# Kernel optimization log

Measured on AMD Instinct MI355X. Metric: run time of the kernel, lower is better.

## Reference

```python
import jax, jax.numpy as jnp
import numpy as np
from functools import partial

BANK = 256
ADDR = 64
OUT_C, IN_C, KH, KW = 64, 64, 3, 3
BS, H, W = 32, 128, 128


def setup_inputs() -> dict:
    key = jax.random.key(0)
    ks = jax.random.split(key, 6)
    x = jax.random.normal(ks[0], (BS, IN_C, H, W), dtype=jnp.float32)
    w_addr = jax.random.normal(ks[1], (BS, ADDR), dtype=jnp.float32)
    b_addr = jax.random.normal(ks[2], (BS, OUT_C, ADDR), dtype=jnp.float32)
    # learned parameters
    w_bank = jax.random.normal(ks[3], (BANK, OUT_C, IN_C, KH, KW), dtype=jnp.float32) * (1.0 / np.sqrt(IN_C * KH * KW))
    bound = 1.0 / np.sqrt(IN_C * KH * KW)
    b_bank = jax.random.uniform(ks[4], (BANK,), minval=-bound, maxval=bound, dtype=jnp.float32)
    address_space = jax.random.normal(ks[5], (BANK, ADDR), dtype=jnp.float32)
    return {"x": x, "w_addr": w_addr, "b_addr": b_addr, "w_bank": w_bank,
            "b_bank": b_bank, "address_space": address_space, "s": 1, "p": 1}


def _hyper_conv(x, w_addr, b_addr, w_bank, b_bank, address_space, s, p):
    # soft addressing: keys @ address_space.T -> softmax -> weighted sum of bank
    sel_w = jax.nn.softmax(w_addr @ address_space.T, axis=-1)          # [bs, bank]
    w = jnp.einsum('bn,noikl->boikl', sel_w, w_bank)                   # [bs, O, I, kh, kw]
    sel_b = jax.nn.softmax(b_addr @ address_space.T, axis=-1)          # [bs, O, bank]
    b = jnp.einsum('bon,n->bo', sel_b, b_bank)                         # [bs, O]

    def conv_one(xi, wi):
        # xi: [I, H, W], wi: [O, I, kh, kw]
        return jax.lax.conv_general_dilated(
            xi[None], wi, window_strides=(s, s), padding=[(p, p), (p, p)],
            dimension_numbers=('NCHW', 'OIHW', 'NCHW'))[0]

    o = jax.vmap(conv_one)(x, w)                                       # [bs, O, H', W']
    return o + b[:, :, None, None]


def reference(x, w_addr, b_addr, w_bank, b_bank, address_space, s, p):
    return _hyper_conv(x, w_addr, b_addr, w_bank, b_bank, address_space, int(s), int(p))
```

## Files before the change

kernel.cpp:

```cpp
#include <hip/hip_runtime.h>
#include <hip/hip_bf16.h>
#include <math.h>

#define BS   32
#define IC   64
#define OC   64
#define HH   128
#define WW   128
#define BANK 256
#define ADDR 64
#define WELEM (OC*IC*9)
#define PLANE (HH*WW)

typedef short short8 __attribute__((ext_vector_type(8)));
typedef float f32x16 __attribute__((ext_vector_type(16)));

__device__ __forceinline__ short f2bf(float f) {
    unsigned u = __builtin_bit_cast(unsigned, f);
    unsigned r = (u + 0x7FFFu + ((u >> 16) & 1u)) >> 16;
    return (short)r;
}

__global__ __launch_bounds__(BANK) void k_selw(const float* __restrict__ w_addr,
                                               const float* __restrict__ aspace,
                                               float* __restrict__ sel_w) {
    int b = blockIdx.x;
    int n = threadIdx.x;
    const float* wa = w_addr + b * ADDR;
    const float* as = aspace + n * ADDR;
    float dot = 0.f;
#pragma unroll
    for (int k = 0; k < ADDR; ++k) dot = fmaf(wa[k], as[k], dot);

    __shared__ float red[BANK];
    red[n] = dot; __syncthreads();
    for (int s = BANK / 2; s > 0; s >>= 1) {
        if (n < s) red[n] = fmaxf(red[n], red[n + s]);
        __syncthreads();
    }
    float m = red[0]; __syncthreads();
    float e = expf(dot - m);
    red[n] = e; __syncthreads();
    for (int s = BANK / 2; s > 0; s >>= 1) {
        if (n < s) red[n] += red[n + s];
        __syncthreads();
    }
    sel_w[b * BANK + n] = e / red[0];
}

__global__ __launch_bounds__(BANK) void k_bias(const float* __restrict__ b_addr,
                                               const float* __restrict__ aspace,
                                               const float* __restrict__ b_bank,
                                               float* __restrict__ bias) {
    int bo = blockIdx.x;
    int n  = threadIdx.x;
    const float* ba = b_addr + (size_t)bo * ADDR;
    const float* as = aspace + n * ADDR;
    float dot = 0.f;
#pragma unroll
    for (int k = 0; k < ADDR; ++k) dot = fmaf(ba[k], as[k], dot);

    __shared__ float red[BANK];
    red[n] = dot; __syncthreads();
    for (int s = BANK / 2; s > 0; s >>= 1) {
        if (n < s) red[n] = fmaxf(red[n], red[n + s]);
        __syncthreads();
    }
    float m = red[0]; __syncthreads();
    float e = expf(dot - m);
    red[n] = e; __syncthreads();
    for (int s = BANK / 2; s > 0; s >>= 1) {
        if (n < s) red[n] += red[n + s];
        __syncthreads();
    }
    float denom = red[0]; __syncthreads();
    red[n] = e * b_bank[n]; __syncthreads();
    for (int s = BANK / 2; s > 0; s >>= 1) {
        if (n < s) red[n] += red[n + s];
        __syncthreads();
    }
    if (n == 0) bias[bo] = red[0] / denom;
}

__global__ __launch_bounds__(256) void k_wmix(const float* __restrict__ sel_w,
                                              const float* __restrict__ w_bank,
                                              __hip_bfloat16* __restrict__ wmb) {
    __shared__ float s_red[4 * 32 * 64];

    int tid = threadIdx.x;
    int jl  = tid & 63;
    int c   = tid >> 6;
    int jb  = blockIdx.x * 64 + jl;

    int n0 = __builtin_amdgcn_readfirstlane(c * 64);
    const float* selp = sel_w + n0;

    float wv[64];
#pragma unroll
    for (int n = 0; n < 64; ++n)
        wv[n] = w_bank[(size_t)(n0 + n) * WELEM + jb];

    float acc[BS];
#pragma unroll
    for (int b = 0; b < BS; ++b) acc[b] = 0.f;
#pragma unroll
    for (int b = 0; b < BS; ++b)
#pragma unroll
        for (int n = 0; n < 64; ++n)
            acc[b] = fmaf(selp[b * BANK + n], wv[n], acc[b]);

#pragma unroll
    for (int b = 0; b < BS; ++b)
        s_red[(c * 32 + b) * 64 + jl] = acc[b];
    __syncthreads();

    int B0  = (tid * 8) & 31;
    int jl2 = (tid * 8) >> 5;
    int j   = blockIdx.x * 64 + jl2;
    int o   = j / 576;
    int rem = j - o * 576;
    int i   = rem / 9;
    int tap = rem - i * 9;
    size_t base = ((size_t)tap * 8 + (i >> 3)) * 512 + (size_t)o * 8 + (i & 7);
#pragma unroll
    for (int u = 0; u < 8; ++u) {
        int b = B0 + u;
        float v = s_red[(0 * 32 + b) * 64 + jl2] + s_red[(1 * 32 + b) * 64 + jl2]
                + s_red[(2 * 32 + b) * 64 + jl2] + s_red[(3 * 32 + b) * 64 + jl2];
        short sv = f2bf(v);
        wmb[(size_t)b * (9 * 8 * 64 * 8) + base] = *reinterpret_cast<__hip_bfloat16*>(&sv);
    }
}

__global__ __launch_bounds__(512, 4) void k_conv(const float* __restrict__ x,
                                                 const short* __restrict__ wmb,
                                                 const float* __restrict__ bias,
                                                 float* __restrict__ out) {
    __shared__ short s_x[2][4 * 2 * 132 * 8];
    __shared__ short s_w[2][9 * 2 * 64 * 8];
    __shared__ float s_bias[OC];

    int orig    = blockIdx.x;
    int logical = (orig & 7) * 256 + (orig >> 3);
    int b    = logical >> 6;
    int y0   = (logical & 63) * 2;
    int tid  = threadIdx.x;
    int lane = tid & 63;
    int wv   = tid >> 6;
    int h    = lane >> 5;
    int ln   = lane & 31;
    int wr   = wv & 1;
    int oh   = (wv >> 1) & 1;
    int ph   = wv >> 2;

    if (tid < OC) s_bias[tid] = bias[b * OC + tid];
    if (tid < 32) {
        int bf   = tid >> 4;
        int kg   = (tid >> 1) & 7;
        int col  = (tid & 1) ? 129 : 0;
        *(short8*)&s_x[bf][(kg * 132 + col) * 8] = (short8){0,0,0,0,0,0,0,0};
    }

    const float* xb   = x + (size_t)b * IC * PLANE;
    const short* wmbs = wmb + (size_t)b * 36864;

    int x_goff[2], x_lds[2]; bool x_ok[2]; int x_g[2];
#pragma unroll
    for (int k = 0; k < 2; ++k) {
        int u  = k * 512 + tid;
        int ky = u >> 8;
        int g  = (u >> 7) & 1;
        int cx = u & 127;
        int gy = y0 - 1 + ky;
        x_ok[k]   = ((unsigned)gy < (unsigned)HH);
        x_g[k]    = g;
        x_goff[k] = gy * WW + cx;
        x_lds[k]  = ((ky * 2 + g) * 132 + cx + 1) * 8;
    }
    bool w_val[3]; int w_tap[3], w_g[3], w_oc[3];
#pragma unroll
    for (int k = 0; k < 3; ++k) {
        int v = k * 512 + tid;
        w_val[k] = (v < 1152);
        int vv = w_val[k] ? v : 0;
        w_tap[k] = vv >> 7; w_g[k] = (vv >> 6) & 1; w_oc[k] = vv & 63;
    }

    float  xr[2][8];
    short8 wreg[3];

    auto LOAD = [&](int cc) {
#pragma unroll
        for (int k = 0; k < 2; ++k) {
            if (x_ok[k]) {
                const float* p = xb + (size_t)(cc * 16 + x_g[k] * 8) * PLANE + x_goff[k];
#pragma unroll
                for (int e = 0; e < 8; ++e) xr[k][e] = p[(size_t)e * PLANE];
            } else {
#pragma unroll
                for (int e = 0; e < 8; ++e) xr[k][e] = 0.f;
            }
        }
#pragma unroll
        for (int k = 0; k < 3; ++k)
            if (w_val[k])
                wreg[k] = *(const short8*)(wmbs +
                    (size_t)((w_tap[k] * 8 + 2 * cc + w_g[k]) * 64 + w_oc[k]) * 8);
    };
    auto STORE = [&](int bf) {
#pragma unroll
        for (int k = 0; k < 2; ++k) {
            short8 s;
#pragma unroll
            for (int e = 0; e < 8; ++e) s[e] = f2bf(xr[k][e]);
            *(short8*)&s_x[bf][x_lds[k]] = s;
        }
#pragma unroll
        for (int k = 0; k < 3; ++k)
            if (w_val[k])
                *(short8*)&s_w[bf][((w_tap[k] * 2 + w_g[k]) * 64 + w_oc[k]) * 8] = wreg[k];
    };

    f32x16 acc[2];
    acc[0] = (f32x16)0.0f;
    acc[1] = (f32x16)0.0f;

    LOAD(0);
    STORE(0);
    __syncthreads();

#pragma unroll
    for (int cc = 0; cc < 4; ++cc) {
        int bf = cc & 1;
        if (cc < 3) LOAD(cc + 1);
        const short8* xb8 = (const short8*)s_x[bf];
        const short8* wb8 = (const short8*)s_w[bf];
#pragma unroll
        for (int ky = 0; ky < 3; ++ky) {
#pragma unroll
            for (int kx = 0; kx < 3; ++kx) {
                short8 a = wb8[((ky * 3 + kx) * 2 + h) * 64 + oh * 32 + ln];
#pragma unroll
                for (int nt = 0; nt < 2; ++nt) {
                    short8 bb = xb8[((wr + ky) * 2 + h) * 132 + ph * 64 + nt * 32 + ln + kx];
                    acc[nt] = __builtin_amdgcn_mfma_f32_32x32x16_bf16(a, bb, acc[nt], 0, 0, 0);
                }
            }
        }
        if (cc < 3) STORE(bf ^ 1);
        __syncthreads();
    }

    int y = y0 + wr;
    float* ob = out + (size_t)b * OC * PLANE;
#pragma unroll
    for (int nt = 0; nt < 2; ++nt) {
#pragma unroll
        for (int r = 0; r < 16; ++r) {
            int oc = oh * 32 + (r & 3) + 8 * (r >> 2) + 4 * h;
            int px = ph * 64 + nt * 32 + ln;
            ob[((size_t)oc * HH + y) * WW + px] = acc[nt][r] + s_bias[oc];
        }
    }
}

extern "C" void kernel_launch(void* const* d_in, const int* in_sizes, int n_in,
                              void* d_out, int out_size, void* d_ws, size_t ws_size,
                              hipStream_t stream) {
    const float* x      = (const float*)d_in[0];
    const float* w_addr = (const float*)d_in[1];
    const float* b_addr = (const float*)d_in[2];
    const float* w_bank = (const float*)d_in[3];
    const float* b_bank = (const float*)d_in[4];
    const float* aspace = (const float*)d_in[5];
    float* out = (float*)d_out;

    char* ws = (char*)d_ws;
    float*          sel_w = (float*)ws;
    float*          bias  = (float*)(ws + 32768);
    __hip_bfloat16* wmb   = (__hip_bfloat16*)(ws + 40960);

    k_selw<<<BS, BANK, 0, stream>>>(w_addr, aspace, sel_w);
    k_bias<<<BS * OC, BANK, 0, stream>>>(b_addr, aspace, b_bank, bias);
    k_wmix<<<WELEM / 64, 256, 0, stream>>>(sel_w, w_bank, wmb);
    k_conv<<<BS * 64, 512, 0, stream>>>(x, (const short*)wmb, bias, out);
}
```

Before: 133.2 us.

## Split conv tiles into half-width blocks with register-held weights and single LDS buffer

The conv kernel now uses 256-thread blocks that each cover two rows and half the image width, launching twice as many blocks. Weight fragments are read straight from global memory into registers per channel chunk instead of being staged in LDS. The double-buffered LDS pipeline is replaced by a single buffer with two barriers per chunk. The aim is to cut LDS use and raise occupancy, at the cost of more halo reloading of x, more redundant weight fetches and loss of load/compute overlap.

```diff
diff --git a/kernel.cpp b/kernel.cpp
--- a/kernel.cpp
+++ b/kernel.cpp
@@ -132,123 +132,104 @@
     }
 }
 
-__global__ __launch_bounds__(512, 4) void k_conv(const float* __restrict__ x,
+__global__ __launch_bounds__(256, 4) void k_conv(const float* __restrict__ x,
                                                  const short* __restrict__ wmb,
                                                  const float* __restrict__ bias,
                                                  float* __restrict__ out) {
-    __shared__ short s_x[2][4 * 2 * 132 * 8];
-    __shared__ short s_w[2][9 * 2 * 64 * 8];
+    __shared__ short s_x[4 * 2 * 66 * 8];
     __shared__ float s_bias[OC];
 
     int orig    = blockIdx.x;
-    int logical = (orig & 7) * 256 + (orig >> 3);
-    int b    = logical >> 6;
-    int y0   = (logical & 63) * 2;
+    int logical = (orig & 7) * 512 + (orig >> 3);
+    int b    = logical >> 7;
+    int rem  = logical & 127;
+    int y0   = (rem >> 1) * 2;
+    int ch   = rem & 1;
     int tid  = threadIdx.x;
     int lane = tid & 63;
     int wv   = tid >> 6;
     int h    = lane >> 5;
     int ln   = lane & 31;
     int wr   = wv & 1;
-    int oh   = (wv >> 1) & 1;
-    int ph   = wv >> 2;
+    int oh   = wv >> 1;
 
     if (tid < OC) s_bias[tid] = bias[b * OC + tid];
-    if (tid < 32) {
-        int bf   = tid >> 4;
-        int kg   = (tid >> 1) & 7;
-        int col  = (tid & 1) ? 129 : 0;
-        *(short8*)&s_x[bf][(kg * 132 + col) * 8] = (short8){0,0,0,0,0,0,0,0};
-    }
 
     const float* xb   = x + (size_t)b * IC * PLANE;
     const short* wmbs = wmb + (size_t)b * 36864;
 
-    int x_goff[2], x_lds[2]; bool x_ok[2]; int x_g[2];
-#pragma unroll
-    for (int k = 0; k < 2; ++k) {
-        int u  = k * 512 + tid;
-        int ky = u >> 8;
-        int g  = (u >> 7) & 1;
-        int cx = u & 127;
+    int x_goff[3], x_lds[3], x_g[3]; bool x_ok[3];
+#pragma unroll
+    for (int k = 0; k < 3; ++k) {
+        int u = k * 256 + tid;
+        bool val = (u < 528);
+        int uu = val ? u : 0;
+        int ky = uu / 132;
+        int r  = uu - ky * 132;
+        int g  = r / 66;
+        int cx = r - g * 66;
         int gy = y0 - 1 + ky;
-        x_ok[k]   = ((unsigned)gy < (unsigned)HH);
+        int gx = ch * 64 - 1 + cx;
+        x_ok[k]   = val && ((unsigned)gy < (unsigned)HH) && ((unsigned)gx < (unsigned)WW);
         x_g[k]    = g;
-        x_goff[k] = gy * WW + cx;
-        x_lds[k]  = ((ky * 2 + g) * 132 + cx + 1) * 8;
-    }
-    bool w_val[3]; int w_tap[3], w_g[3], w_oc[3];
-#pragma unroll
-    for (int k = 0; k < 3; ++k) {
-        int v = k * 512 + tid;
-        w_val[k] = (v < 1152);
-        int vv = w_val[k] ? v : 0;
-        w_tap[k] = vv >> 7; w_g[k] = (vv >> 6) & 1; w_oc[k] = vv & 63;
-    }
-
-    float  xr[2][8];
-    short8 wreg[3];
-
-    auto LOAD = [&](int cc) {
-#pragma unroll
-        for (int k = 0; k < 2; ++k) {
-            if (x_ok[k]) {
-                const float* p = xb + (size_t)(cc * 16 + x_g[k] * 8) * PLANE + x_goff[k];
-#pragma unroll
-                for (int e = 0; e < 8; ++e) xr[k][e] = p[(size_t)e * PLANE];
-            } else {
-#pragma unroll
-                for (int e = 0; e < 8; ++e) xr[k][e] = 0.f;
-            }
-        }
-#pragma unroll
-        for (int k = 0; k < 3; ++k)
-            if (w_val[k])
-                wreg[k] = *(const short8*)(wmbs +
-                    (size_t)((w_tap[k] * 8 + 2 * cc + w_g[k]) * 64 + w_oc[k]) * 8);
-    };
-    auto STORE = [&](int bf) {
-#pragma unroll
-        for (int k = 0; k < 2; ++k) {
-            short8 s;
-#pragma unroll
-            for (int e = 0; e < 8; ++e) s[e] = f2bf(xr[k][e]);
-            *(short8*)&s_x[bf][x_lds[k]] = s;
-        }
-#pragma unroll
-        for (int k = 0; k < 3; ++k)
-            if (w_val[k])
-                *(short8*)&s_w[bf][((w_tap[k] * 2 + w_g[k]) * 64 + w_oc[k]) * 8] = wreg[k];
-    };
+        x_goff[k] = gy * WW + gx;
+        x_lds[k]  = val ? ((ky * 2 + g) * 66 + cx) * 8 : (528 * 8);
+        if (!val) x_lds[k] = 0;
+        if (!val) x_ok[k] = false;
+    }
+    bool x_val[3];
+#pragma unroll
+    for (int k = 0; k < 3; ++k) x_val[k] = (k * 256 + tid) < 528;
 
     f32x16 acc[2];
     acc[0] = (f32x16)0.0f;
     acc[1] = (f32x16)0.0f;
 
-    LOAD(0);
-    STORE(0);
-    __syncthreads();
-
-#pragma unroll
+    const short8* sx8 = (const short8*)s_x;
+
     for (int cc = 0; cc < 4; ++cc) {
-        int bf = cc & 1;
-        if (cc < 3) LOAD(cc + 1);
-        const short8* xb8 = (const short8*)s_x[bf];
-        const short8* wb8 = (const short8*)s_w[bf];
+        short8 areg[9];
+#pragma unroll
+        for (int tap = 0; tap < 9; ++tap)
+            areg[tap] = *(const short8*)(wmbs +
+                (size_t)((tap * 8 + 2 * cc + h) * 64 + oh * 32 + ln) * 8);
+
+        float xr[3][8];
+#pragma unroll
+        for (int k = 0; k < 3; ++k) {
+            if (x_ok[k]) {
+                const float* p = xb + (size_t)(cc * 16 + x_g[k] * 8) * PLANE + x_goff[k];
+#pragma unroll
+                for (int e = 0; e < 8; ++e) xr[k][e] = p[(size_t)e * PLANE];
+            } else {
+#pragma unroll
+                for (int e = 0; e < 8; ++e) xr[k][e] = 0.f;
+            }
+        }
+        if (cc) __syncthreads();
+#pragma unroll
+        for (int k = 0; k < 3; ++k) {
+            if (x_val[k]) {
+                short8 s;
+#pragma unroll
+                for (int e = 0; e < 8; ++e) s[e] = f2bf(xr[k][e]);
+                *(short8*)&s_x[x_lds[k]] = s;
+            }
+        }
+        __syncthreads();
+
 #pragma unroll
         for (int ky = 0; ky < 3; ++ky) {
 #pragma unroll
             for (int kx = 0; kx < 3; ++kx) {
-                short8 a = wb8[((ky * 3 + kx) * 2 + h) * 64 + oh * 32 + ln];
+                short8 a = areg[ky * 3 + kx];
 #pragma unroll
                 for (int nt = 0; nt < 2; ++nt) {
-                    short8 bb = xb8[((wr + ky) * 2 + h) * 132 + ph * 64 + nt * 32 + ln + kx];
+                    short8 bb = sx8[((wr + ky) * 2 + h) * 66 + nt * 32 + ln + kx];
                     acc[nt] = __builtin_amdgcn_mfma_f32_32x32x16_bf16(a, bb, acc[nt], 0, 0, 0);
                 }
             }
         }
-        if (cc < 3) STORE(bf ^ 1);
-        __syncthreads();
     }
 
     int y = y0 + wr;
@@ -258,7 +239,7 @@
 #pragma unroll
         for (int r = 0; r < 16; ++r) {
             int oc = oh * 32 + (r & 3) + 8 * (r >> 2) + 4 * h;
-            int px = ph * 64 + nt * 32 + ln;
+            int px = ch * 64 + nt * 32 + ln;
             ob[((size_t)oc * HH + y) * WW + px] = acc[nt][r] + s_bias[oc];
         }
     }
@@ -283,5 +264,5 @@
     k_selw<<<BS, BANK, 0, stream>>>(w_addr, aspace, sel_w);
     k_bias<<<BS * OC, BANK, 0, stream>>>(b_addr, aspace, b_bank, bias);
     k_wmix<<<WELEM / 64, 256, 0, stream>>>(sel_w, w_bank, wmb);
-    k_conv<<<BS * 64, 512, 0, stream>>>(x, (const short*)wmb, bias, out);
-}
+    k_conv<<<BS * 64 * 2, 256, 0, stream>>>(x, (const short*)wmb, bias, out);
+}
```

New measurement: 150.2 us. 12.8% more time.
